# Optimization experiments

Hardware: AMD Instinct MI355X
Metric: run time of the kernel (lower is better)

The kernel has to match this reference:

```python
import jax, jax.numpy as jnp
import numpy as np

N_NODES = 100000
N_EDGES = 1600000
D = 64
N_LAYERS = 6  # 3 KAN blocks x 2 KANLinear
GRID_SIZE = 5
SPLINE_ORDER = 3
N_COEF = GRID_SIZE + SPLINE_ORDER  # 8


def _grid():
    # uniform B-spline grid on [-1, 1], extended by spline_order on each side
    h = 2.0 / GRID_SIZE
    return (jnp.arange(-SPLINE_ORDER, GRID_SIZE + SPLINE_ORDER + 1, dtype=jnp.float32) * h - 1.0)  # [G+2k+1]=12


def b_splines(x):
    # x: [N, D] -> bases [N, D, G+k] via Cox-de Boor recursion
    grid = _grid()
    xe = x[..., None]  # [N, D, 1]
    b = ((xe >= grid[:-1]) & (xe < grid[1:])).astype(x.dtype)  # order-0, [N,D,G+2k]
    for p in range(1, SPLINE_ORDER + 1):
        left = (xe - grid[: -(p + 1)]) / (grid[p:-1] - grid[: -(p + 1)])
        right = (grid[p + 1:] - xe) / (grid[p + 1:] - grid[1:-p])
        b = left * b[..., :-1] + right * b[..., 1:]
    return b  # [N, D, N_COEF]


def kan_linear(x, bw, sw, ss):
    # efficient-KAN layer: SiLU base branch + B-spline branch with standalone scaler
    base = jax.nn.silu(x) @ bw.T                      # [N, O]
    bas = b_splines(x)                                # [N, D, K]
    spline = jnp.einsum('ndk,odk->no', bas, sw * ss[..., None])
    return base + spline


def spmm(edge_row, edge_col, edge_val, x):
    # out[i] = sum_{(i,j) in E} val * x[j]  -- COO sparse-dense matmul
    msgs = edge_val[:, None] * x[edge_col]            # [E, D] gather
    return jax.ops.segment_sum(msgs, edge_row, num_segments=N_NODES)


def setup_inputs() -> dict:
    key = jax.random.key(0)
    ks = jax.random.split(key, 7)
    x = jax.random.uniform(ks[0], (N_NODES, D), jnp.float32, -1.0, 1.0)
    edge_row = jnp.sort(jax.random.randint(ks[1], (N_EDGES,), 0, N_NODES))
    edge_col = jax.random.randint(ks[2], (N_EDGES,), 0, N_NODES)
    edge_val = jax.random.uniform(ks[3], (N_EDGES,), jnp.float32, 0.0, 1.0) * (1.0 / 16.0)
    base_w = jax.random.normal(ks[4], (N_LAYERS, D, D), jnp.float32) * (1.0 / np.sqrt(D))
    spline_w = jax.random.normal(ks[5], (N_LAYERS, D, D, N_COEF), jnp.float32) * 0.1
    spline_s = jax.random.normal(ks[6], (N_LAYERS, D, D), jnp.float32) * (1.0 / np.sqrt(D))
    return {"x": x, "edge_val": edge_val, "base_w": base_w, "spline_w": spline_w,
            "spline_s": spline_s, "edge_row": edge_row, "edge_col": edge_col}


def reference(x, edge_val, base_w, spline_w, spline_s, edge_row, edge_col):
    idx = 0
    for _block in range(3):          # mp_layers = 3 KAN blocks
        x = spmm(edge_row, edge_col, edge_val, x)
        for _l in range(2):          # kan_layers = 2 KANLinear per block
            x = kan_linear(x, base_w[idx], spline_w[idx], spline_s[idx])
            idx += 1
    return x
```

## Files before the change

### kernel.cpp

```cpp
#include <hip/hip_runtime.h>
#include <math.h>

#define N_NODES 100000
#define N_EDGES 1600000
#define DIM 64
#define N_LAYERS 6
#define N_COEF 8
#define NSTEP 18
#define NTILE 16
#define KAN_BLOCKS (N_NODES / NTILE)

typedef _Float16 f16x8 __attribute__((ext_vector_type(8)));
typedef _Float16 f16x4 __attribute__((ext_vector_type(4)));
typedef float f32x4 __attribute__((ext_vector_type(4)));

__device__ __forceinline__ unsigned f16u(float v) {
    return (unsigned)__builtin_bit_cast(unsigned short, (_Float16)v);
}

__global__ void build_wcf(const float* __restrict__ bw,
                          const float* __restrict__ sw,
                          const float* __restrict__ ss,
                          uint4* __restrict__ wcf) {
    int idx = blockIdx.x * blockDim.x + threadIdx.x;
    if (idx >= N_LAYERS * NSTEP * 4 * 64) return;
    int lane = idx & 63;
    int nt   = (idx >> 6) & 3;
    int s    = (idx >> 8) % NSTEP;
    int l    = idx / (64 * 4 * NSTEP);
    int o = nt * 16 + (lane & 15);

    unsigned short h[8];
#pragma unroll
    for (int j = 0; j < 8; ++j) {
        int k = s * 32 + ((lane >> 4) << 3) + j;
        int d = k / 9;
        int r = k - d * 9;
        float v;
        if (r == 0) v = bw[(l * DIM + o) * DIM + d];
        else        v = sw[((l * DIM + o) * DIM + d) * N_COEF + (r - 1)] *
                        ss[(l * DIM + o) * DIM + d];
        h[j] = __builtin_bit_cast(unsigned short, (_Float16)v);
    }
    uint4 uh;
    uh.x = (unsigned)h[0] | ((unsigned)h[1] << 16);
    uh.y = (unsigned)h[2] | ((unsigned)h[3] << 16);
    uh.z = (unsigned)h[4] | ((unsigned)h[5] << 16);
    uh.w = (unsigned)h[6] | ((unsigned)h[7] << 16);
    wcf[((l * NSTEP + s) * 4 + nt) * 64 + lane] = uh;
}

__global__ void build_rowptr(const int* __restrict__ erow, int* __restrict__ rp) {
    int i = blockIdx.x * blockDim.x + threadIdx.x;
    if (i > N_NODES) return;
    if (i == N_NODES) { rp[i] = N_EDGES; return; }
    int a = 0, b = N_EDGES;
    while (a < b) { int m = (a + b) >> 1; if (erow[m] < i) a = m + 1; else b = m; }
    rp[i] = a;
}

__global__ void conv_f16(const float* __restrict__ in, _Float16* __restrict__ out) {
    int i = blockIdx.x * blockDim.x + threadIdx.x;
    float4 v = *(const float4*)(in + (size_t)i * 4);
    f16x4 h = { (_Float16)v.x, (_Float16)v.y, (_Float16)v.z, (_Float16)v.w };
    *(f16x4*)(out + (size_t)i * 4) = h;
}

#define META4(C, V, E)                                                  \
    { int e_ = (E) + q; if (e_ < end) { C = ecol[e_]; V = ev[e_]; }     \
      else { C = 0; V = 0.f; } }

__global__ __launch_bounds__(256) void spmm_kernel(const int* __restrict__ rp,
                                                   const int* __restrict__ ecol,
                                                   const float* __restrict__ ev,
                                                   const _Float16* __restrict__ x,
                                                   _Float16* __restrict__ y) {
    int wid = (blockIdx.x * blockDim.x + threadIdx.x) >> 6;
    int lane = threadIdx.x & 63;
    if (wid >= N_NODES) return;
    int q = lane >> 4;
    int c16 = lane & 15;
    int e0 = rp[wid], end = rp[wid + 1];

    float4 acc = {0.f, 0.f, 0.f, 0.f};
    int c0 = 0, c1 = 0; float v0 = 0.f, v1 = 0.f;
    if (e0 < end) { META4(c0, v0, e0) META4(c1, v1, e0 + 4) }

    for (int eb = e0; eb < end; eb += 8) {
        int n0 = 0, n1 = 0; float w0 = 0.f, w1 = 0.f;
        if (eb + 8 < end) { META4(n0, w0, eb + 8) META4(n1, w1, eb + 12) }
        f16x4 g0 = *(const f16x4*)&x[(size_t)c0 * DIM + c16 * 4];
        f16x4 g1 = *(const f16x4*)&x[(size_t)c1 * DIM + c16 * 4];
        acc.x += v0 * (float)g0[0]; acc.y += v0 * (float)g0[1];
        acc.z += v0 * (float)g0[2]; acc.w += v0 * (float)g0[3];
        acc.x += v1 * (float)g1[0]; acc.y += v1 * (float)g1[1];
        acc.z += v1 * (float)g1[2]; acc.w += v1 * (float)g1[3];
        c0 = n0; v0 = w0; c1 = n1; v1 = w1;
    }

    acc.x += __shfl_xor(acc.x, 16); acc.y += __shfl_xor(acc.y, 16);
    acc.z += __shfl_xor(acc.z, 16); acc.w += __shfl_xor(acc.w, 16);
    acc.x += __shfl_xor(acc.x, 32); acc.y += __shfl_xor(acc.y, 32);
    acc.z += __shfl_xor(acc.z, 32); acc.w += __shfl_xor(acc.w, 32);

    if (lane < 16) {
        f16x4 h = { (_Float16)acc.x, (_Float16)acc.y, (_Float16)acc.z, (_Float16)acc.w };
        *(f16x4*)&y[(size_t)wid * DIM + c16 * 4] = h;
    }
}

__device__ __forceinline__ void spline_window(float xv, unsigned long long& lo,
                                              unsigned long long& hi) {
    float t = xv * 2.5f + 5.5f;
    float fl = floorf(t);
    float u = t - fl;
    int c = (int)fl;
    bool valid = (t >= 0.f) && (t < 11.f);
    float u2 = u * u, u3 = u2 * u, um = 1.f - u;
    const float k6 = 1.f / 6.f;
    float N0 = um * um * um * k6;
    float N1 = (3.f * u3 - 6.f * u2 + 4.f) * k6;
    float N2 = (-3.f * u3 + 3.f * u2 + 3.f * u + 1.f) * k6;
    float N3 = u3 * k6;
    if (!valid) { N0 = 0.f; N1 = 0.f; N2 = 0.f; N3 = 0.f; }
    unsigned n01 = f16u(N0) | (f16u(N1) << 16);
    unsigned n23 = f16u(N2) | (f16u(N3) << 16);
    unsigned long long big = (unsigned long long)n01 | ((unsigned long long)n23 << 32);
    int qb = c - 3;
    qb = qb < -3 ? -3 : (qb > 7 ? 7 : qb);
    int sh = qb * 16;
    lo = 0; hi = 0;
    if (sh >= 0) {
        if (sh < 64) { lo = big << sh; hi = (big >> 1) >> (63 - sh); }
        else         { hi = big << (sh - 64); }
    } else {
        lo = big >> (-sh);
    }
}

__device__ __forceinline__ void feat_pair(char* lds, int lbase, int Xsw, int d,
                                          float xe, float xo) {
    float se_f = xe * __builtin_amdgcn_rcpf(1.f + __expf(-xe));
    float so_f = xo * __builtin_amdgcn_rcpf(1.f + __expf(-xo));
    unsigned se = f16u(se_f), so = f16u(so_f);

    unsigned long long loE, hiE, loO, hiO;
    spline_window(xe, loE, hiE);
    spline_window(xo, loO, hiO);

    unsigned wv[9];
    wv[0] = se | ((unsigned)loE << 16);
    wv[1] = (unsigned)(loE >> 16);
    wv[2] = (unsigned)(loE >> 48) | ((unsigned)hiE << 16);
    wv[3] = (unsigned)(hiE >> 16);
    wv[4] = (unsigned)(hiE >> 48) | (so << 16);
    wv[5] = (unsigned)loO;
    wv[6] = (unsigned)(loO >> 32);
    wv[7] = (unsigned)hiO;
    wv[8] = (unsigned)(hiO >> 32);

    int base = lbase + 18 * d;
#pragma unroll
    for (int j = 0; j < 9; ++j)
        *(unsigned*)(&lds[(base + 4 * j) ^ Xsw]) = wv[j];
}

template<int F32OUT>
__global__ __launch_bounds__(256, 4) void kan_mfma(const _Float16* __restrict__ xin,
                                                   const uint4* __restrict__ wl,
                                                   void* __restrict__ outp) {
    __shared__ alignas(16) char lds[NTILE * 1152];

    int tid = threadIdx.x;
    int lane = tid & 63;
    int w = tid >> 6;
    int node0 = blockIdx.x * NTILE;

    int fn = tid >> 4;
    int fq = tid & 15;
    int Xsw = (fn & 7) << 4;
    int lbase = fn * 1152;
    {
        f16x4 hv = *(const f16x4*)&xin[(size_t)(node0 + fn) * DIM + fq * 4];
        int d0 = fq * 4;
        feat_pair(lds, lbase, Xsw, d0,     (float)hv[0], (float)hv[1]);
        feat_pair(lds, lbase, Xsw, d0 + 2, (float)hv[2], (float)hv[3]);
    }
    __syncthreads();

    int row = lane & 15, kg = lane >> 4;
    int xr = (row & 7) << 4;
    int rb = row * 1152;

    f32x4 acc = {0.f, 0.f, 0.f, 0.f};
#pragma unroll
    for (int s = 0; s < NSTEP; ++s) {
        f16x8 bh = __builtin_bit_cast(f16x8, wl[(s * 4 + w) * 64 + lane]);
        int pofs = ((s * 4 + kg) << 4) ^ xr;
        f16x8 a = *(const f16x8*)(&lds[rb + pofs]);
        acc = __builtin_amdgcn_mfma_f32_16x16x32_f16(a, bh, acc, 0, 0, 0);
    }

    int o = w * 16 + row;
    int rbase = kg * 4;
    if (F32OUT) {
        float* out = (float*)outp;
#pragma unroll
        for (int r = 0; r < 4; ++r)
            out[(size_t)(node0 + rbase + r) * DIM + o] = acc[r];
    } else {
        _Float16* out = (_Float16*)outp;
#pragma unroll
        for (int r = 0; r < 4; ++r)
            out[(size_t)(node0 + rbase + r) * DIM + o] = (_Float16)acc[r];
    }
}

extern "C" void kernel_launch(void* const* d_in, const int* in_sizes, int n_in,
                              void* d_out, int out_size, void* d_ws, size_t ws_size,
                              hipStream_t stream) {
    const float* x     = (const float*)d_in[0];
    const float* eval_ = (const float*)d_in[1];
    const float* bw    = (const float*)d_in[2];
    const float* sw    = (const float*)d_in[3];
    const float* ss    = (const float*)d_in[4];
    const int*   erow  = (const int*)d_in[5];
    const int*   ecol  = (const int*)d_in[6];
    float* out = (float*)d_out;

    const size_t HB = (size_t)N_NODES * DIM * sizeof(_Float16);
    _Float16* H0 = (_Float16*)d_ws;
    _Float16* H1 = (_Float16*)((char*)d_ws + HB);
    uint4* wcf = (uint4*)((char*)d_ws + 2 * HB);
    int*   rp  = (int*)((char*)d_ws + 2 * HB + 442368);

    const size_t WL = (size_t)NSTEP * 4 * 64;

    build_wcf<<<(N_LAYERS * NSTEP * 4 * 64 + 255) / 256, 256, 0, stream>>>(bw, sw, ss, wcf);
    build_rowptr<<<(N_NODES + 256) / 256, 256, 0, stream>>>(erow, rp);
    conv_f16<<<(N_NODES * DIM / 4 + 255) / 256, 256, 0, stream>>>(x, H0);

    const int SPMM_BLOCKS = N_NODES / 4;

    spmm_kernel<<<SPMM_BLOCKS, 256, 0, stream>>>(rp, ecol, eval_, H0, H1);
    kan_mfma<0><<<KAN_BLOCKS, 256, 0, stream>>>(H1, wcf + 0 * WL, H1);
    kan_mfma<0><<<KAN_BLOCKS, 256, 0, stream>>>(H1, wcf + 1 * WL, H0);

    spmm_kernel<<<SPMM_BLOCKS, 256, 0, stream>>>(rp, ecol, eval_, H0, H1);
    kan_mfma<0><<<KAN_BLOCKS, 256, 0, stream>>>(H1, wcf + 2 * WL, H1);
    kan_mfma<0><<<KAN_BLOCKS, 256, 0, stream>>>(H1, wcf + 3 * WL, H0);

    spmm_kernel<<<SPMM_BLOCKS, 256, 0, stream>>>(rp, ecol, eval_, H0, H1);
    kan_mfma<0><<<KAN_BLOCKS, 256, 0, stream>>>(H1, wcf + 4 * WL, H1);
    kan_mfma<1><<<KAN_BLOCKS, 256, 0, stream>>>(H1, wcf + 5 * WL, out);
}
```

Measured before the change: 284.2 us.

## Widen SpMM edge batching to 16 and double KAN node tile to 32

The SpMM loop now prefetches edge metadata 16 at a time and issues four row gathers per iteration, where it used to issue two. This raises memory-level parallelism on the random gathers. The KAN MFMA kernel now handles 32 nodes per block with two accumulators, so each weight fragment loaded from global memory feeds two MFMAs, halving weight traffic per node. In exchange, LDS use per block doubles, more registers are needed, the occupancy hint in launch_bounds is removed, and the block count is halved.

```diff
diff --git a/kernel.cpp b/kernel.cpp
--- a/kernel.cpp
+++ b/kernel.cpp
@@ -7,7 +7,7 @@
 #define N_LAYERS 6
 #define N_COEF 8
 #define NSTEP 18
-#define NTILE 16
+#define NTILE 32
 #define KAN_BLOCKS (N_NODES / NTILE)
 
 typedef _Float16 f16x8 __attribute__((ext_vector_type(8)));
@@ -66,9 +66,13 @@
     *(f16x4*)(out + (size_t)i * 4) = h;
 }
 
-#define META4(C, V, E)                                                  \
-    { int e_ = (E) + q; if (e_ < end) { C = ecol[e_]; V = ev[e_]; }     \
-      else { C = 0; V = 0.f; } }
+#define META16(C, V, BASE)                                              \
+    _Pragma("unroll")                                                   \
+    for (int i_ = 0; i_ < 4; ++i_) {                                    \
+        int e_ = (BASE) + 4 * i_ + q;                                   \
+        if (e_ < end) { C[i_] = ecol[e_]; V[i_] = ev[e_]; }             \
+        else          { C[i_] = 0;        V[i_] = 0.f; }                \
+    }
 
 __global__ __launch_bounds__(256) void spmm_kernel(const int* __restrict__ rp,
                                                    const int* __restrict__ ecol,
@@ -83,19 +87,26 @@
     int e0 = rp[wid], end = rp[wid + 1];
 
     float4 acc = {0.f, 0.f, 0.f, 0.f};
-    int c0 = 0, c1 = 0; float v0 = 0.f, v1 = 0.f;
-    if (e0 < end) { META4(c0, v0, e0) META4(c1, v1, e0 + 4) }
-
-    for (int eb = e0; eb < end; eb += 8) {
-        int n0 = 0, n1 = 0; float w0 = 0.f, w1 = 0.f;
-        if (eb + 8 < end) { META4(n0, w0, eb + 8) META4(n1, w1, eb + 12) }
-        f16x4 g0 = *(const f16x4*)&x[(size_t)c0 * DIM + c16 * 4];
-        f16x4 g1 = *(const f16x4*)&x[(size_t)c1 * DIM + c16 * 4];
-        acc.x += v0 * (float)g0[0]; acc.y += v0 * (float)g0[1];
-        acc.z += v0 * (float)g0[2]; acc.w += v0 * (float)g0[3];
-        acc.x += v1 * (float)g1[0]; acc.y += v1 * (float)g1[1];
-        acc.z += v1 * (float)g1[2]; acc.w += v1 * (float)g1[3];
-        c0 = n0; v0 = w0; c1 = n1; v1 = w1;
+    int ca[4]; float va[4];
+    int cb[4]; float vb[4];
+    META16(ca, va, e0)
+
+    for (int eb = e0; eb < end; eb += 16) {
+        META16(cb, vb, eb + 16)
+        f16x4 g0 = *(const f16x4*)&x[(size_t)ca[0] * DIM + c16 * 4];
+        f16x4 g1 = *(const f16x4*)&x[(size_t)ca[1] * DIM + c16 * 4];
+        f16x4 g2 = *(const f16x4*)&x[(size_t)ca[2] * DIM + c16 * 4];
+        f16x4 g3 = *(const f16x4*)&x[(size_t)ca[3] * DIM + c16 * 4];
+        acc.x += va[0] * (float)g0[0]; acc.y += va[0] * (float)g0[1];
+        acc.z += va[0] * (float)g0[2]; acc.w += va[0] * (float)g0[3];
+        acc.x += va[1] * (float)g1[0]; acc.y += va[1] * (float)g1[1];
+        acc.z += va[1] * (float)g1[2]; acc.w += va[1] * (float)g1[3];
+        acc.x += va[2] * (float)g2[0]; acc.y += va[2] * (float)g2[1];
+        acc.z += va[2] * (float)g2[2]; acc.w += va[2] * (float)g2[3];
+        acc.x += va[3] * (float)g3[0]; acc.y += va[3] * (float)g3[1];
+        acc.z += va[3] * (float)g3[2]; acc.w += va[3] * (float)g3[3];
+#pragma unroll
+        for (int i_ = 0; i_ < 4; ++i_) { ca[i_] = cb[i_]; va[i_] = vb[i_]; }
     }
 
     acc.x += __shfl_xor(acc.x, 16); acc.y += __shfl_xor(acc.y, 16);
@@ -166,9 +177,9 @@
 }
 
 template<int F32OUT>
-__global__ __launch_bounds__(256, 4) void kan_mfma(const _Float16* __restrict__ xin,
-                                                   const uint4* __restrict__ wl,
-                                                   void* __restrict__ outp) {
+__global__ __launch_bounds__(256) void kan_mfma(const _Float16* __restrict__ xin,
+                                                const uint4* __restrict__ wl,
+                                                void* __restrict__ outp) {
     __shared__ alignas(16) char lds[NTILE * 1152];
 
     int tid = threadIdx.x;
@@ -176,29 +187,37 @@
     int w = tid >> 6;
     int node0 = blockIdx.x * NTILE;
 
-    int fn = tid >> 4;
-    int fq = tid & 15;
+    int fn = tid >> 3;
+    int fq = tid & 7;
     int Xsw = (fn & 7) << 4;
     int lbase = fn * 1152;
     {
-        f16x4 hv = *(const f16x4*)&xin[(size_t)(node0 + fn) * DIM + fq * 4];
+        const _Float16* xr_ = &xin[(size_t)(node0 + fn) * DIM + fq * 4];
+        f16x4 h0 = *(const f16x4*)(xr_);
+        f16x4 h1 = *(const f16x4*)(xr_ + 32);
         int d0 = fq * 4;
-        feat_pair(lds, lbase, Xsw, d0,     (float)hv[0], (float)hv[1]);
-        feat_pair(lds, lbase, Xsw, d0 + 2, (float)hv[2], (float)hv[3]);
+        feat_pair(lds, lbase, Xsw, d0,          (float)h0[0], (float)h0[1]);
+        feat_pair(lds, lbase, Xsw, d0 + 2,      (float)h0[2], (float)h0[3]);
+        feat_pair(lds, lbase, Xsw, d0 + 32,     (float)h1[0], (float)h1[1]);
+        feat_pair(lds, lbase, Xsw, d0 + 32 + 2, (float)h1[2], (float)h1[3]);
     }
     __syncthreads();
 
     int row = lane & 15, kg = lane >> 4;
     int xr = (row & 7) << 4;
-    int rb = row * 1152;
-
-    f32x4 acc = {0.f, 0.f, 0.f, 0.f};
+    int rb0 = row * 1152;
+    int rb1 = (16 + row) * 1152;
+
+    f32x4 acc0 = {0.f, 0.f, 0.f, 0.f};
+    f32x4 acc1 = {0.f, 0.f, 0.f, 0.f};
 #pragma unroll
     for (int s = 0; s < NSTEP; ++s) {
         f16x8 bh = __builtin_bit_cast(f16x8, wl[(s * 4 + w) * 64 + lane]);
         int pofs = ((s * 4 + kg) << 4) ^ xr;
-        f16x8 a = *(const f16x8*)(&lds[rb + pofs]);
-        acc = __builtin_amdgcn_mfma_f32_16x16x32_f16(a, bh, acc, 0, 0, 0);
+        f16x8 a0 = *(const f16x8*)(&lds[rb0 + pofs]);
+        f16x8 a1 = *(const f16x8*)(&lds[rb1 + pofs]);
+        acc0 = __builtin_amdgcn_mfma_f32_16x16x32_f16(a0, bh, acc0, 0, 0, 0);
+        acc1 = __builtin_amdgcn_mfma_f32_16x16x32_f16(a1, bh, acc1, 0, 0, 0);
     }
 
     int o = w * 16 + row;
@@ -206,13 +225,17 @@
     if (F32OUT) {
         float* out = (float*)outp;
 #pragma unroll
-        for (int r = 0; r < 4; ++r)
-            out[(size_t)(node0 + rbase + r) * DIM + o] = acc[r];
+        for (int r = 0; r < 4; ++r) {
+            out[(size_t)(node0 + rbase + r) * DIM + o]      = acc0[r];
+            out[(size_t)(node0 + 16 + rbase + r) * DIM + o] = acc1[r];
+        }
     } else {
         _Float16* out = (_Float16*)outp;
 #pragma unroll
-        for (int r = 0; r < 4; ++r)
-            out[(size_t)(node0 + rbase + r) * DIM + o] = (_Float16)acc[r];
+        for (int r = 0; r < 4; ++r) {
+            out[(size_t)(node0 + rbase + r) * DIM + o]      = (_Float16)acc0[r];
+            out[(size_t)(node0 + 16 + rbase + r) * DIM + o] = (_Float16)acc1[r];
+        }
     }
 }
 
```

Measured after the change: 272.4 us. -4.2%, faster.
